# Optimization experiments

Hardware: AMD Instinct MI355X
Metric: run time of the kernel (lower is better)

## Reference

```python
import jax, jax.numpy as jnp
import numpy as np

SCALE = 1.0 / np.sqrt(256.0)  # 1/sqrt(hidden_dim)


def setup_inputs() -> dict:
    key = jax.random.key(0)
    ks = jax.random.split(key, 9)
    N, C, H, W = 32, 256, 32, 32
    D, T = 256, 512
    s = lambda k, shape, fan: jax.random.normal(k, shape, jnp.float32) / np.sqrt(fan)
    return {
        "x": jax.random.normal(ks[0], (N, C, H, W), jnp.float32),
        "t": jax.random.normal(ks[1], (N, T), jnp.float32),
        "W_t": s(ks[2], (C, T), T),
        "b_t": jnp.zeros((C,), jnp.float32),
        "Wq": s(ks[3], (D, C), C),
        "Wk": s(ks[4], (D, C), C),
        "Wv": s(ks[5], (D, C), C),
        "Wp": s(ks[6], (C, D), D),
        "bp": jnp.zeros((C,), jnp.float32),
    }


def reference(x, t, W_t, b_t, Wq, Wk, Wv, Wp, bp):
    N, C, H, W = x.shape
    h = x
    # time embedding: Linear + ReLU, broadcast over spatial dims
    temb = jax.nn.relu(t @ W_t.T + b_t)  # [N, C]
    x = x + temb[:, :, None, None]
    # transpose(1,3): [N, C, H, W] -> [N, W, H, C]
    xc = jnp.transpose(x, (0, 3, 2, 1))
    q = xc @ Wq.T  # [N, W, H, D]
    k = xc @ Wk.T
    v = xc @ Wv.T
    # full spatial attention scores: [N, W, H, w, h]
    qk = jnp.einsum('NWHd,Nwhd->NWHwh', q, k) * SCALE
    qk = jax.nn.softmax(qk.reshape(N, W, H, W * H), axis=-1)
    qk = qk.reshape(N, W, H, W, H)
    out = jnp.einsum('NWHwh,Nwhd->NWHd', qk, v)  # [N, W, H, D]
    out = out @ Wp.T + bp  # [N, W, H, C]
    out = jnp.transpose(out, (0, 3, 2, 1))  # [N, C, H, W]
    return out + h
```

## Files before the change

kernel.cpp:

```cpp
#include <hip/hip_runtime.h>
#include <hip/hip_bf16.h>

#define NB 32
#define CD 256
#define SS 1024
#define DD 256
#define TT 512
#define QSCALE 0.09016844f

typedef __attribute__((ext_vector_type(8))) short s16x8;
typedef __attribute__((ext_vector_type(4))) short s16x4;
typedef __attribute__((ext_vector_type(4))) float f32x4;
typedef __attribute__((ext_vector_type(16))) float f32x16;
typedef __attribute__((ext_vector_type(4))) unsigned int u32x4;

__device__ __forceinline__ unsigned short f2bf(float f) {
  unsigned u = __builtin_bit_cast(unsigned, f);
  u = (u + 0x7FFFu + ((u >> 16) & 1u)) >> 16;
  return (unsigned short)u;
}
__device__ __forceinline__ float bf2f(unsigned short h) {
  return __builtin_bit_cast(float, ((unsigned)h) << 16);
}
__device__ __forceinline__ unsigned pk2(float a, float b) {
  float2 f2; f2.x = a; f2.y = b;
  __hip_bfloat162 h = __float22bfloat162_rn(f2);
  unsigned u;
  __builtin_memcpy(&u, &h, 4);
  return u;
}
__device__ __forceinline__ float asf(unsigned u) {
  return __builtin_bit_cast(float, u);
}
#define GLOAD16(gp, lp)                                                        \
  __builtin_amdgcn_global_load_lds(                                            \
      (const __attribute__((address_space(1))) unsigned int*)(const void*)(gp),\
      (__attribute__((address_space(3))) unsigned int*)(void*)(lp), 16, 0, 0)

__global__ __launch_bounds__(256) void k_misc(const float* __restrict__ t,
    const float* __restrict__ Wt, const float* __restrict__ bt, float* __restrict__ temb,
    const float* __restrict__ wq, const float* __restrict__ wk,
    const float* __restrict__ wv, const float* __restrict__ wp,
    unsigned short* __restrict__ dst) {
  const int b = blockIdx.x;
  if (b < 1024) {
    const int i = b * 256 + threadIdx.x;
    const int which = i >> 16, off = i & 65535;
    const float* s = which == 0 ? wq : which == 1 ? wk : which == 2 ? wv : wp;
    dst[i] = f2bf(s[off]);
  } else {
    const int n = b - 1024, c = threadIdx.x;
    const float4* tv = (const float4*)(t + (size_t)n * TT);
    const float4* wvv = (const float4*)(Wt + (size_t)c * TT);
    float acc = 0.f;
#pragma unroll 8
    for (int i = 0; i < TT / 4; ++i) {
      float4 a = tv[i], bb = wvv[i];
      acc += a.x * bb.x + a.y * bb.y + a.z * bb.z + a.w * bb.w;
    }
    acc += bt[c];
    temb[n * CD + c] = fmaxf(acc, 0.f);
  }
}

__global__ __launch_bounds__(256) void k_addT(const float* __restrict__ x,
    const float* __restrict__ temb, unsigned short* __restrict__ xb) {
  __shared__ float tile[32][33];
  const int tx = threadIdx.x & 31, ty = threadIdx.x >> 5;
  const int n = blockIdx.z, s0 = blockIdx.y * 32, c0 = blockIdx.x * 32;
#pragma unroll
  for (int i = 0; i < 4; ++i) {
    const int cc = ty + i * 8;
    tile[cc][tx] = x[((size_t)n * CD + c0 + cc) * SS + s0 + tx] + temb[n * CD + c0 + cc];
  }
  __syncthreads();
  unsigned short* op = xb + ((size_t)n * SS + s0) * CD + c0;
#pragma unroll
  for (int i = 0; i < 4; ++i) {
    const int ss = ty + i * 8;
    op[(size_t)ss * CD + tx] = f2bf(tile[tx][ss]);
  }
}

__global__ __launch_bounds__(256) void k_qkv(const unsigned short* __restrict__ A,
    const unsigned short* __restrict__ wb, unsigned short* __restrict__ qb,
    unsigned short* __restrict__ kb, unsigned short* __restrict__ vtb) {
  __shared__ __attribute__((aligned(16))) unsigned short As[128 * 32];
  __shared__ __attribute__((aligned(16))) unsigned short Bs[128 * 32];
  const int bid = blockIdx.x;
  const int xcd = bid & 7, idx = bid >> 3;
  const int n = xcd + 8 * (idx / 48);
  const int rem = idx % 48;
  const int which = rem >> 4, tt = rem & 15;
  const int s0 = (tt & 7) * 128;
  const int d0 = (tt >> 3) * 128;
  const unsigned short* B = wb + which * 65536;
  const int tid = threadIdx.x;
  const int lane = tid & 63, wid = tid >> 6;
  const int lo = lane & 15, hi = lane >> 4;
  const int wr = wid >> 1, wc = wid & 1;
  const unsigned short* An = A + (size_t)n * SS * CD;
  f32x4 acc[4][4] = {};
  for (int k0 = 0; k0 < CD; k0 += 32) {
#pragma unroll
    for (int i = 0; i < 2; ++i) {
      const int seg = i * 256 + wid * 64 + lane;
      const int row = seg >> 2, c8 = seg & 3;
      GLOAD16(An + (size_t)(s0 + row) * CD + k0 + c8 * 8, As + (size_t)(i * 256 + wid * 64) * 8);
      GLOAD16(B + (size_t)(d0 + row) * CD + k0 + c8 * 8, Bs + (size_t)(i * 256 + wid * 64) * 8);
    }
    __syncthreads();
    s16x8 a[4], b[4];
#pragma unroll
    for (int mi = 0; mi < 4; ++mi)
      a[mi] = *(const s16x8*)&As[(wr * 64 + mi * 16 + lo) * 32 + hi * 8];
#pragma unroll
    for (int ni = 0; ni < 4; ++ni)
      b[ni] = *(const s16x8*)&Bs[(wc * 64 + ni * 16 + lo) * 32 + hi * 8];
#pragma unroll
    for (int mi = 0; mi < 4; ++mi)
#pragma unroll
      for (int ni = 0; ni < 4; ++ni)
        acc[mi][ni] = __builtin_amdgcn_mfma_f32_16x16x32_bf16(a[mi], b[ni], acc[mi][ni], 0, 0, 0);
    __syncthreads();
  }
  if (which < 2) {
    const float osc = which == 0 ? QSCALE : 1.0f;
    unsigned short* On = (which == 0 ? qb : kb) + (size_t)n * SS * DD;
#pragma unroll
    for (int mi = 0; mi < 4; ++mi) {
      const int r0 = s0 + wr * 64 + mi * 16 + hi * 4;
#pragma unroll
      for (int ni = 0; ni < 4; ++ni) {
        const int col = d0 + wc * 64 + ni * 16 + lo;
#pragma unroll
        for (int r = 0; r < 4; ++r)
          On[(size_t)(r0 + r) * DD + col] = f2bf(acc[mi][ni][r] * osc);
      }
    }
  } else {
    unsigned short* On = vtb + (size_t)n * DD * SS;
#pragma unroll
    for (int mi = 0; mi < 4; ++mi) {
      const int r0 = s0 + wr * 64 + mi * 16 + hi * 4;
#pragma unroll
      for (int ni = 0; ni < 4; ++ni) {
        const int col = d0 + wc * 64 + ni * 16 + lo;
        s16x4 v;
#pragma unroll
        for (int r = 0; r < 4; ++r) v[r] = (short)f2bf(acc[mi][ni][r]);
        *(s16x4*)&On[(size_t)col * SS + r0] = v;
      }
    }
  }
}

__global__ __launch_bounds__(256, 2) void k_attn(const unsigned short* __restrict__ qb,
    const unsigned short* __restrict__ kb, const unsigned short* __restrict__ vtb,
    unsigned short* __restrict__ ob) {
  __shared__ __attribute__((aligned(16))) unsigned short lds[24576];
  const int bid = blockIdx.x;
  const int xcd = bid & 7, inner = bid >> 3;
  const int n = xcd + ((inner >> 4) << 3);
  const int sub = inner & 15;
  const int qt = sub & 7, dh = sub >> 3;
  const int tid = threadIdx.x, lane = tid & 63, w = tid >> 6;
  const int l31 = lane & 31, h = lane >> 5;
  const int dblk = dh * 128;
  const unsigned short* Kn = kb + (size_t)n * SS * DD;
  const unsigned short* Vn = vtb + ((size_t)n * DD + dblk) * SS;
  const int qrow = qt * 128 + w * 32 + l31;

  const unsigned short* Qp = qb + ((size_t)n * SS + qrow) * DD + h * 8;
  s16x8 qf[16];
#pragma unroll
  for (int ks = 0; ks < 16; ++ks) qf[ks] = *(const s16x8*)(Qp + ks * 16);

  f32x16 acc[4] = {};
  float lrun = 0.f;

  auto STAGE = [&](int buf, int jt) {
    const int j0 = jt * 32;
    unsigned short* KsB = lds + buf * 8192;
    unsigned short* VsB = lds + 16384 + buf * 4096;
#pragma unroll
    for (int i = 0; i < 4; ++i) {
      const int idx = i * 256 + w * 64 + lane;
      const int row = idx >> 5, c8 = idx & 31;
      GLOAD16(Kn + (size_t)(j0 + row) * DD + ((c8 ^ (row & 7)) << 3),
              KsB + (size_t)(i * 256 + w * 64) * 8);
    }
#pragma unroll
    for (int i = 0; i < 2; ++i) {
      const int idx = i * 256 + w * 64 + lane;
      const int row = idx >> 2, c8 = idx & 3;
      GLOAD16(Vn + (size_t)row * SS + j0 + ((c8 ^ ((row >> 1) & 3)) << 3),
              VsB + (size_t)(i * 256 + w * 64) * 8);
    }
  };

  STAGE(0, 0);
  __syncthreads();

  int cur = 0;
#pragma unroll 1
  for (int jt = 0; jt < 32; ++jt) {
    if (jt + 1 < 32) STAGE(cur ^ 1, jt + 1);
    const unsigned short* Ks = lds + cur * 8192;
    const unsigned short* Vs = lds + 16384 + cur * 4096;
    f32x16 sca = {}, scb = {};
    __builtin_amdgcn_s_setprio(1);
#pragma unroll
    for (int ks = 0; ks < 16; ks += 2) {
      const s16x8 kfa = *(const s16x8*)&Ks[l31 * 256 + ((((ks * 2 + h)) ^ (l31 & 7)) << 3)];
      const s16x8 kfb = *(const s16x8*)&Ks[l31 * 256 + (((((ks + 1) * 2 + h)) ^ (l31 & 7)) << 3)];
      sca = __builtin_amdgcn_mfma_f32_32x32x16_bf16(kfa, qf[ks], sca, 0, 0, 0);
      scb = __builtin_amdgcn_mfma_f32_32x32x16_bf16(kfb, qf[ks + 1], scb, 0, 0, 0);
    }
    __builtin_amdgcn_s_setprio(0);
    f32x16 sc = sca + scb;
#pragma unroll
    for (int i = 0; i < 16; ++i) sc[i] = exp2f(sc[i]);
    lrun += (((sc[0] + sc[1]) + (sc[2] + sc[3])) + ((sc[4] + sc[5]) + (sc[6] + sc[7]))) +
            (((sc[8] + sc[9]) + (sc[10] + sc[11])) + ((sc[12] + sc[13]) + (sc[14] + sc[15])));
    const unsigned wv0 = pk2(sc[0], sc[1]),   wv1 = pk2(sc[2], sc[3]);
    const unsigned wv2 = pk2(sc[4], sc[5]),   wv3 = pk2(sc[6], sc[7]);
    const unsigned wv4 = pk2(sc[8], sc[9]),   wv5 = pk2(sc[10], sc[11]);
    const unsigned wv6 = pk2(sc[12], sc[13]), wv7 = pk2(sc[14], sc[15]);
    auto r02 = __builtin_amdgcn_permlane32_swap(wv0, wv2, false, false);
    auto r13 = __builtin_amdgcn_permlane32_swap(wv1, wv3, false, false);
    auto r46 = __builtin_amdgcn_permlane32_swap(wv4, wv6, false, false);
    auto r57 = __builtin_amdgcn_permlane32_swap(wv5, wv7, false, false);
    const u32x4 pa0u = {r02[0], r13[0], r02[1], r13[1]};
    const u32x4 pa1u = {r46[0], r57[0], r46[1], r57[1]};
    const s16x8 pa0 = __builtin_bit_cast(s16x8, pa0u);
    const s16x8 pa1 = __builtin_bit_cast(s16x8, pa1u);
    __builtin_amdgcn_s_setprio(1);
#pragma unroll
    for (int dc = 0; dc < 4; ++dc) {
      const s16x8 vf0 = *(const s16x8*)&Vs[(dc * 32 + l31) * 32 + ((h ^ ((l31 >> 1) & 3)) << 3)];
      acc[dc] = __builtin_amdgcn_mfma_f32_32x32x16_bf16(vf0, pa0, acc[dc], 0, 0, 0);
    }
#pragma unroll
    for (int dc = 0; dc < 4; ++dc) {
      const s16x8 vf1 = *(const s16x8*)&Vs[(dc * 32 + l31) * 32 + (((2 + h) ^ ((l31 >> 1) & 3)) << 3)];
      acc[dc] = __builtin_amdgcn_mfma_f32_32x32x16_bf16(vf1, pa1, acc[dc], 0, 0, 0);
    }
    __builtin_amdgcn_s_setprio(0);
    __syncthreads();
    cur ^= 1;
  }
  {
    auto rl = __builtin_amdgcn_permlane32_swap(__builtin_bit_cast(unsigned, lrun),
                                               __builtin_bit_cast(unsigned, lrun), false, false);
    lrun = asf(rl[0]) + asf(rl[1]);
  }
  const float inv = 1.0f / lrun;
  unsigned short* Op = ob + ((size_t)n * SS + qrow) * DD + dblk;
#pragma unroll
  for (int dc = 0; dc < 4; ++dc)
#pragma unroll
    for (int rg = 0; rg < 4; ++rg) {
      uint2 u;
      u.x = pk2(acc[dc][rg * 4 + 0] * inv, acc[dc][rg * 4 + 1] * inv);
      u.y = pk2(acc[dc][rg * 4 + 2] * inv, acc[dc][rg * 4 + 3] * inv);
      *(uint2*)(Op + dc * 32 + rg * 8 + h * 4) = u;
    }
}

__global__ __launch_bounds__(256) void k_proj(const unsigned short* __restrict__ ob,
    const unsigned short* __restrict__ wpb, const float* __restrict__ bp,
    const float* __restrict__ x, float* __restrict__ out) {
  __shared__ __attribute__((aligned(16))) unsigned short As[128 * 32];
  __shared__ __attribute__((aligned(16))) unsigned short Bs[128 * 32];
  const int bid = blockIdx.x;
  const int xcd = bid & 7, idx = bid >> 3;
  const int n = xcd + ((idx >> 4) << 3);
  const int rem = idx & 15;
  const int s0 = (rem & 7) * 128;
  const int c0 = (rem >> 3) * 128;
  const int tid = threadIdx.x;
  const int lane = tid & 63, wid = tid >> 6;
  const int lo = lane & 15, hi = lane >> 4;
  const int wr = wid >> 1, wc = wid & 1;
  const unsigned short* On = ob + (size_t)n * SS * DD;
  f32x4 acc[4][4] = {};
  for (int k0 = 0; k0 < DD; k0 += 32) {
#pragma unroll
    for (int i = 0; i < 2; ++i) {
      const int seg = i * 256 + wid * 64 + lane;
      const int row = seg >> 2, c8 = seg & 3;
      GLOAD16(wpb + (size_t)(c0 + row) * DD + k0 + c8 * 8, As + (size_t)(i * 256 + wid * 64) * 8);
      GLOAD16(On + (size_t)(s0 + row) * DD + k0 + c8 * 8, Bs + (size_t)(i * 256 + wid * 64) * 8);
    }
    __syncthreads();
    s16x8 a[4], b[4];
#pragma unroll
    for (int mi = 0; mi < 4; ++mi)
      a[mi] = *(const s16x8*)&As[(wr * 64 + mi * 16 + lo) * 32 + hi * 8];
#pragma unroll
    for (int ni = 0; ni < 4; ++ni)
      b[ni] = *(const s16x8*)&Bs[(wc * 64 + ni * 16 + lo) * 32 + hi * 8];
#pragma unroll
    for (int mi = 0; mi < 4; ++mi)
#pragma unroll
      for (int ni = 0; ni < 4; ++ni)
        acc[mi][ni] = __builtin_amdgcn_mfma_f32_16x16x32_bf16(a[mi], b[ni], acc[mi][ni], 0, 0, 0);
    __syncthreads();
  }
#pragma unroll
  for (int mi = 0; mi < 4; ++mi) {
#pragma unroll
    for (int r = 0; r < 4; ++r) {
      const int c = c0 + wr * 64 + mi * 16 + hi * 4 + r;
      const float bpc = bp[c];
      const size_t base = ((size_t)n * CD + c) * SS;
#pragma unroll
      for (int ni = 0; ni < 4; ++ni) {
        const int s = s0 + wc * 64 + ni * 16 + lo;
        out[base + s] = acc[mi][ni][r] + bpc + x[base + s];
      }
    }
  }
}

extern "C" void kernel_launch(void* const* d_in, const int* in_sizes, int n_in,
                              void* d_out, int out_size, void* d_ws, size_t ws_size,
                              hipStream_t stream) {
  const float* x  = (const float*)d_in[0];
  const float* t  = (const float*)d_in[1];
  const float* Wt = (const float*)d_in[2];
  const float* bt = (const float*)d_in[3];
  const float* Wq = (const float*)d_in[4];
  const float* Wk = (const float*)d_in[5];
  const float* Wv = (const float*)d_in[6];
  const float* Wp = (const float*)d_in[7];
  const float* bp = (const float*)d_in[8];
  char* ws = (char*)d_ws;
  float* temb        = (float*)ws;
  unsigned short* wb = (unsigned short*)(ws + 32768);
  unsigned short* xb = (unsigned short*)(ws + 557056);
  unsigned short* qb = (unsigned short*)(ws + 17334272);
  unsigned short* kb = (unsigned short*)(ws + 34111488);
  unsigned short* vtb = (unsigned short*)(ws + 50888704);
  unsigned short* ob = (unsigned short*)(ws + 67665920);
  float* out = (float*)d_out;

  k_misc<<<1056, 256, 0, stream>>>(t, Wt, bt, temb, Wq, Wk, Wv, Wp, wb);
  k_addT<<<dim3(8, 32, 32), 256, 0, stream>>>(x, temb, xb);
  k_qkv<<<1536, 256, 0, stream>>>(xb, wb, qb, kb, vtb);
  k_attn<<<512, 256, 0, stream>>>(qb, kb, vtb, ob);
  k_proj<<<512, 256, 0, stream>>>(ob, wb + 196608, bp, x, out);
}
```

Baseline: 142.8 us.

## Software-pipeline attention loop: triple-buffer K/V and overlap next QK with current PV

Moves the attention loop from a two-stage to a three-stage LDS ring, prefetching two tiles ahead. The QK^T scores for the next tile are computed before the exp/pack/PV work of the current tile, so score MFMAs can overlap the softmax VALU work. It also drops the split dual accumulator in favour of one chained accumulator, and switches to the raw exp2 builtin. LDS use rises to 72KB per block, which may limit occupancy to two blocks per CU, and the extra live score registers add pressure under the launch bound.

```diff
diff --git a/kernel.cpp b/kernel.cpp
--- a/kernel.cpp
+++ b/kernel.cpp
@@ -158,7 +158,7 @@
 __global__ __launch_bounds__(256, 2) void k_attn(const unsigned short* __restrict__ qb,
     const unsigned short* __restrict__ kb, const unsigned short* __restrict__ vtb,
     unsigned short* __restrict__ ob) {
-  __shared__ __attribute__((aligned(16))) unsigned short lds[24576];
+  __shared__ __attribute__((aligned(16))) unsigned short lds[36864];
   const int bid = blockIdx.x;
   const int xcd = bid & 7, inner = bid >> 3;
   const int n = xcd + ((inner >> 4) << 3);
@@ -182,7 +182,7 @@
   auto STAGE = [&](int buf, int jt) {
     const int j0 = jt * 32;
     unsigned short* KsB = lds + buf * 8192;
-    unsigned short* VsB = lds + 16384 + buf * 4096;
+    unsigned short* VsB = lds + 24576 + buf * 4096;
 #pragma unroll
     for (int i = 0; i < 4; ++i) {
       const int idx = i * 256 + w * 64 + lane;
@@ -200,33 +200,39 @@
   };
 
   STAGE(0, 0);
+  STAGE(1, 1);
   __syncthreads();
 
-  int cur = 0;
+  f32x16 scc = {};
+#pragma unroll
+  for (int ks = 0; ks < 16; ++ks) {
+    const s16x8 kf = *(const s16x8*)&lds[l31 * 256 + ((((ks * 2 + h)) ^ (l31 & 7)) << 3)];
+    scc = __builtin_amdgcn_mfma_f32_32x32x16_bf16(kf, qf[ks], scc, 0, 0, 0);
+  }
+
+  int sb = 2, qkb = 1, pvb = 0;
 #pragma unroll 1
-  for (int jt = 0; jt < 32; ++jt) {
-    if (jt + 1 < 32) STAGE(cur ^ 1, jt + 1);
-    const unsigned short* Ks = lds + cur * 8192;
-    const unsigned short* Vs = lds + 16384 + cur * 4096;
-    f32x16 sca = {}, scb = {};
-    __builtin_amdgcn_s_setprio(1);
-#pragma unroll
-    for (int ks = 0; ks < 16; ks += 2) {
-      const s16x8 kfa = *(const s16x8*)&Ks[l31 * 256 + ((((ks * 2 + h)) ^ (l31 & 7)) << 3)];
-      const s16x8 kfb = *(const s16x8*)&Ks[l31 * 256 + (((((ks + 1) * 2 + h)) ^ (l31 & 7)) << 3)];
-      sca = __builtin_amdgcn_mfma_f32_32x32x16_bf16(kfa, qf[ks], sca, 0, 0, 0);
-      scb = __builtin_amdgcn_mfma_f32_32x32x16_bf16(kfb, qf[ks + 1], scb, 0, 0, 0);
-    }
-    __builtin_amdgcn_s_setprio(0);
-    f32x16 sc = sca + scb;
-#pragma unroll
-    for (int i = 0; i < 16; ++i) sc[i] = exp2f(sc[i]);
-    lrun += (((sc[0] + sc[1]) + (sc[2] + sc[3])) + ((sc[4] + sc[5]) + (sc[6] + sc[7]))) +
-            (((sc[8] + sc[9]) + (sc[10] + sc[11])) + ((sc[12] + sc[13]) + (sc[14] + sc[15])));
-    const unsigned wv0 = pk2(sc[0], sc[1]),   wv1 = pk2(sc[2], sc[3]);
-    const unsigned wv2 = pk2(sc[4], sc[5]),   wv3 = pk2(sc[6], sc[7]);
-    const unsigned wv4 = pk2(sc[8], sc[9]),   wv5 = pk2(sc[10], sc[11]);
-    const unsigned wv6 = pk2(sc[12], sc[13]), wv7 = pk2(sc[14], sc[15]);
+  for (int t = 0; t < 32; ++t) {
+    if (t + 2 < 32) STAGE(sb, t + 2);
+    f32x16 scn = {};
+    if (t + 1 < 32) {
+      const unsigned short* Ks = lds + qkb * 8192;
+      __builtin_amdgcn_s_setprio(1);
+#pragma unroll
+      for (int ks = 0; ks < 16; ++ks) {
+        const s16x8 kf = *(const s16x8*)&Ks[l31 * 256 + ((((ks * 2 + h)) ^ (l31 & 7)) << 3)];
+        scn = __builtin_amdgcn_mfma_f32_32x32x16_bf16(kf, qf[ks], scn, 0, 0, 0);
+      }
+      __builtin_amdgcn_s_setprio(0);
+    }
+#pragma unroll
+    for (int i = 0; i < 16; ++i) scc[i] = __builtin_amdgcn_exp2f(scc[i]);
+    lrun += (((scc[0] + scc[1]) + (scc[2] + scc[3])) + ((scc[4] + scc[5]) + (scc[6] + scc[7]))) +
+            (((scc[8] + scc[9]) + (scc[10] + scc[11])) + ((scc[12] + scc[13]) + (scc[14] + scc[15])));
+    const unsigned wv0 = pk2(scc[0], scc[1]),   wv1 = pk2(scc[2], scc[3]);
+    const unsigned wv2 = pk2(scc[4], scc[5]),   wv3 = pk2(scc[6], scc[7]);
+    const unsigned wv4 = pk2(scc[8], scc[9]),   wv5 = pk2(scc[10], scc[11]);
+    const unsigned wv6 = pk2(scc[12], scc[13]), wv7 = pk2(scc[14], scc[15]);
     auto r02 = __builtin_amdgcn_permlane32_swap(wv0, wv2, false, false);
     auto r13 = __builtin_amdgcn_permlane32_swap(wv1, wv3, false, false);
     auto r46 = __builtin_amdgcn_permlane32_swap(wv4, wv6, false, false);
@@ -235,6 +241,7 @@
     const u32x4 pa1u = {r46[0], r57[0], r46[1], r57[1]};
     const s16x8 pa0 = __builtin_bit_cast(s16x8, pa0u);
     const s16x8 pa1 = __builtin_bit_cast(s16x8, pa1u);
+    const unsigned short* Vs = lds + 24576 + pvb * 4096;
     __builtin_amdgcn_s_setprio(1);
 #pragma unroll
     for (int dc = 0; dc < 4; ++dc) {
@@ -248,7 +255,10 @@
     }
     __builtin_amdgcn_s_setprio(0);
     __syncthreads();
-    cur ^= 1;
+    scc = scn;
+    sb = (sb + 1 == 3) ? 0 : sb + 1;
+    qkb = (qkb + 1 == 3) ? 0 : qkb + 1;
+    pvb = (pvb + 1 == 3) ? 0 : pvb + 1;
   }
   {
     auto rl = __builtin_amdgcn_permlane32_swap(__builtin_bit_cast(unsigned, lrun),
```

Result: faster. 136.1 us (-4.7%).
